# Kernel optimization log

Measured on AMD Instinct MI355X. Metric: run time of the kernel, lower is better.

## Reference

```python
import jax, jax.numpy as jnp
import numpy as np

S, D = 4096, 2048  # seq_len, embedding_space == qkv_dim


def setup_inputs() -> dict:
    key = jax.random.key(0)
    k1, k2, k3, k4, k5 = jax.random.split(key, 5)
    return {
        "input_embedding": jax.random.normal(k1, (S, D), dtype=jnp.float32),
        "query_embedding": jax.random.normal(k2, (S, D), dtype=jnp.float32),
        "Wq": jax.random.normal(k3, (D, D), dtype=jnp.float32) * 0.02,
        "Wk": jax.random.normal(k4, (D, D), dtype=jnp.float32) * 0.02,
        "Wv": jax.random.normal(k5, (D, D), dtype=jnp.float32) * 0.02,
        "include_mask": 0,  # False -> causal mask applied (module's inverted logic)
    }


def reference(input_embedding, query_embedding, Wq, Wk, Wv, include_mask):
    q = query_embedding @ Wq          # [S, D]
    k = input_embedding @ Wk          # [S, D]
    v = input_embedding @ Wv          # [S, D]
    scores = (q @ k.T) / 10.0         # [S, S]; module hardcodes /10, not sqrt(d)
    if not include_mask:
        # causal: -inf strictly above the diagonal (triu with offset 1)
        s = scores.shape[0]
        causal = jnp.tril(jnp.ones((s, s), dtype=bool))
        scores = jnp.where(causal, scores, -jnp.inf)
    probs = jax.nn.softmax(scores, axis=-1)
    return probs @ v                  # [S, D]
```

## Files before the change

kernel.cpp:

```cpp
#include <hip/hip_runtime.h>
#include <hip/hip_bf16.h>
#include <math.h>

typedef __bf16 bf16_t;
typedef __bf16 bf16x8 __attribute__((ext_vector_type(8)));
typedef float f32x4 __attribute__((ext_vector_type(4)));

enum { EP_BF16 = 0, EP_SCORES = 1, EP_F32 = 2 };

__device__ __forceinline__ void gload_lds16(const void* g, void* l) {
  __builtin_amdgcn_global_load_lds(
      (const __attribute__((address_space(1))) void*)g,
      (__attribute__((address_space(3))) void*)l, 16, 0, 0);
}


template <int TM, bool STG>
__device__ __forceinline__ void do_tile(char* smem, int slot, int sslot, size_t stoff,
                                        const char* const* gbase, const int* lbase,
                                        const int* aoff, const int* boff,
                                        f32x4 (&acc)[TM][4]) {
  bf16x8 bfr[4], af[4];
  if constexpr (TM == 8) {
    if constexpr (STG) {
      gload_lds16(gbase[0] + stoff, smem + sslot + lbase[0]);
      gload_lds16(gbase[1] + stoff, smem + sslot + lbase[1]);
    }
#pragma unroll
    for (int n = 0; n < 4; ++n) bfr[n] = *(const bf16x8*)(smem + slot + boff[n]);
#pragma unroll
    for (int m = 0; m < 4; ++m) af[m] = *(const bf16x8*)(smem + slot + aoff[m]);
    __builtin_amdgcn_s_setprio(1);
#pragma unroll
    for (int m = 0; m < 4; ++m)
#pragma unroll
      for (int n = 0; n < 4; ++n)
        acc[m][n] = __builtin_amdgcn_mfma_f32_16x16x32_bf16(af[m], bfr[n], acc[m][n], 0, 0, 0);
    __builtin_amdgcn_s_setprio(0);
    if constexpr (STG) __builtin_amdgcn_s_barrier();
    if constexpr (STG) {
      gload_lds16(gbase[2] + stoff, smem + sslot + lbase[2]);
      gload_lds16(gbase[3] + stoff, smem + sslot + lbase[3]);
    }
#pragma unroll
    for (int m = 0; m < 4; ++m) af[m] = *(const bf16x8*)(smem + slot + aoff[4 + m]);
    __builtin_amdgcn_s_setprio(1);
#pragma unroll
    for (int m = 0; m < 4; ++m)
#pragma unroll
      for (int n = 0; n < 4; ++n)
        acc[4 + m][n] = __builtin_amdgcn_mfma_f32_16x16x32_bf16(af[m], bfr[n], acc[4 + m][n], 0, 0, 0);
    __builtin_amdgcn_s_setprio(0);
  } else {
    if constexpr (STG) {
      gload_lds16(gbase[0] + stoff, smem + sslot + lbase[0]);
      gload_lds16(gbase[1] + stoff, smem + sslot + lbase[1]);
      gload_lds16(gbase[2] + stoff, smem + sslot + lbase[2]);
    }
#pragma unroll
    for (int n = 0; n < 4; ++n) bfr[n] = *(const bf16x8*)(smem + slot + boff[n]);
#pragma unroll
    for (int m = 0; m < 4; ++m) af[m] = *(const bf16x8*)(smem + slot + aoff[m]);
    __builtin_amdgcn_s_setprio(1);
#pragma unroll
    for (int m = 0; m < 4; ++m)
#pragma unroll
      for (int n = 0; n < 4; ++n)
        acc[m][n] = __builtin_amdgcn_mfma_f32_16x16x32_bf16(af[m], bfr[n], acc[m][n], 0, 0, 0);
    __builtin_amdgcn_s_setprio(0);
  }
}

template <int TM, int EPI>
__device__ __forceinline__ void gemm_core(
    const bf16_t* __restrict__ A, const bf16_t* __restrict__ B,
    void* __restrict__ Cout, int M, int N, int K,
    int row0, int col0, bool causal, float scale, char* smem)
{
  constexpr int BM = TM * 32;
  constexpr int LPT_A = BM / 128;
  constexpr int LPT = LPT_A + 2;
  constexpr int ABYTES = BM * 64;
  constexpr int SLOT = (BM + 256) * 64;

  const int tid = threadIdx.x;
  const int w = tid >> 6, lane = tid & 63;
  const int wr = w >> 2, wc = w & 3;

  int Keff = K;
  if (EPI == EP_F32 && causal) Keff = min(K, row0 + BM);
  const int nt = Keff >> 5;

  const char* gbase[LPT];
  int lbase[LPT];
  {
    const int sd = (tid & 3) ^ ((tid >> 3) & 3);
    const int rrow = tid >> 2;
#pragma unroll
    for (int r = 0; r < LPT; ++r) {
      const bool isA = (r < LPT_A);
      const int rr = isA ? r : (r - LPT_A);
      const int R = rr * 128 + rrow;
      const int grow = (isA ? row0 : col0) + R;
      const bf16_t* op = isA ? A : B;
      gbase[r] = (const char*)(op + (size_t)grow * K) + sd * 16;
      lbase[r] = (isA ? 0 : ABYTES) + rr * 8192 + w * 1024;
    }
  }

  const int fl = lane & 15;
  const int arow_off = fl * 64 + (((lane >> 4) ^ ((fl >> 1) & 3)) * 16);
  int aoff[TM], boff[4];
#pragma unroll
  for (int m = 0; m < TM; ++m) aoff[m] = (wr * (TM * 16) + m * 16) * 64 + arow_off;
#pragma unroll
  for (int n = 0; n < 4; ++n) boff[n] = ABYTES + (wc * 64 + n * 16) * 64 + arow_off;

  f32x4 acc[TM][4] = {};

  const int npro = nt < 3 ? nt : 3;
  for (int t = 0; t < npro; ++t)
#pragma unroll
    for (int r = 0; r < LPT; ++r)
      gload_lds16(gbase[r] + (size_t)t * 64, smem + (t & 3) * SLOT + lbase[r]);

  const int nmain = nt - 3;
  for (int t = 0; t < nmain; ++t) {
    if constexpr (TM == 8) asm volatile("s_waitcnt vmcnt(8)" ::: "memory");
    else                   asm volatile("s_waitcnt vmcnt(6)" ::: "memory");
    __builtin_amdgcn_s_barrier();
    asm volatile("" ::: "memory");
    __builtin_amdgcn_sched_barrier(0);
    do_tile<TM, true>(smem, (t & 3) * SLOT, ((t + 3) & 3) * SLOT,
                      (size_t)(t + 3) * 64, gbase, lbase, aoff, boff, acc);
  }

  asm volatile("s_waitcnt vmcnt(0)" ::: "memory");
  __builtin_amdgcn_s_barrier();
  asm volatile("" ::: "memory");
  __builtin_amdgcn_sched_barrier(0);
  for (int t = nmain > 0 ? nmain : 0; t < nt; ++t)
    do_tile<TM, false>(smem, (t & 3) * SLOT, 0, 0, gbase, lbase, aoff, boff, acc);

  const int cr = (lane >> 4) * 4;
  const int cc = lane & 15;
#pragma unroll
  for (int m = 0; m < TM; ++m) {
#pragma unroll
    for (int n = 0; n < 4; ++n) {
#pragma unroll
      for (int i = 0; i < 4; ++i) {
        const int r = row0 + wr * (TM * 16) + m * 16 + cr + i;
        const int c = col0 + wc * 64 + n * 16 + cc;
        float v = acc[m][n][i];
        if (EPI == EP_BF16) {
          ((bf16_t*)Cout)[(size_t)r * N + c] = (bf16_t)v;
        } else if (EPI == EP_SCORES) {
          v *= scale;
          if (causal && c > r) v = -INFINITY;
          ((float*)Cout)[(size_t)r * N + c] = v;
        } else {
          ((float*)Cout)[(size_t)r * N + c] = v;
        }
      }
    }
  }
}

template <int TM, int EPI>
__launch_bounds__(512, 2)
__global__ void gemm_k(const bf16_t* __restrict__ A, const bf16_t* __restrict__ B,
                       void* __restrict__ C, int M, int N, int K,
                       const int* __restrict__ maskflag, float scale) {
  extern __shared__ __align__(16) char smem[];
  const bool causal = (maskflag != nullptr) && (maskflag[0] == 0);
  constexpr int BM = TM * 32;
  const int ntn = N >> 8;
  const int wg = blockIdx.x;
  const int row0 = (wg / ntn) * BM, col0 = (wg % ntn) * 256;
  if (EPI == EP_SCORES && causal && col0 > row0 + BM - 1) return;
  gemm_core<TM, EPI>(A, B, C, M, N, K, row0, col0, causal, scale, smem);
}

__launch_bounds__(512, 2)
__global__ void qkv_k(const bf16_t* __restrict__ qe, const bf16_t* __restrict__ ie,
                      const bf16_t* __restrict__ WqT, const bf16_t* __restrict__ WkT,
                      const bf16_t* __restrict__ WvT,
                      bf16_t* __restrict__ q16, bf16_t* __restrict__ k16,
                      bf16_t* __restrict__ vT16) {
  extern __shared__ __align__(16) char smem[];
  int wg = blockIdx.x;
  const bf16_t *A, *B; bf16_t* C; int M, N;
  if (wg < 128)      { A = qe;  B = WqT; C = q16;  M = 4096; N = 2048; }
  else if (wg < 256) { A = ie;  B = WkT; C = k16;  M = 4096; N = 2048; wg -= 128; }
  else               { A = WvT; B = ie;  C = vT16; M = 2048; N = 4096; wg -= 256; }
  const int ntn = N >> 8;
  const int row0 = (wg / ntn) * 256, col0 = (wg % ntn) * 256;
  gemm_core<8, EP_BF16>(A, B, C, M, N, 2048, row0, col0, false, 1.f, smem);
}


__global__ void cvt_f32_bf16(const float* __restrict__ x, bf16_t* __restrict__ y, long n) {
  long i = ((long)blockIdx.x * blockDim.x + threadIdx.x) * 8;
  const long stride = (long)gridDim.x * blockDim.x * 8;
  for (; i < n; i += stride) {
    const float4 a = *(const float4*)(x + i);
    const float4 b = *(const float4*)(x + i + 4);
    bf16x8 o;
    o[0] = (__bf16)a.x; o[1] = (__bf16)a.y; o[2] = (__bf16)a.z; o[3] = (__bf16)a.w;
    o[4] = (__bf16)b.x; o[5] = (__bf16)b.y; o[6] = (__bf16)b.z; o[7] = (__bf16)b.w;
    *(bf16x8*)(y + i) = o;
  }
}

__global__ void transpose_cvt(const float* __restrict__ W, bf16_t* __restrict__ WT, int Dm) {
  __shared__ float tile[32][33];
  const int bx = blockIdx.x, by = blockIdx.y;
  const int tx = threadIdx.x & 31, ty = threadIdx.x >> 5;
#pragma unroll
  for (int r = ty; r < 32; r += 8)
    tile[r][tx] = W[(size_t)(by * 32 + r) * Dm + bx * 32 + tx];
  __syncthreads();
#pragma unroll
  for (int r = ty; r < 32; r += 8)
    WT[(size_t)(bx * 32 + r) * Dm + by * 32 + tx] = (bf16_t)tile[tx][r];
}

__global__ void softmax_rows(const float* __restrict__ Sc, bf16_t* __restrict__ P,
                             int n, const int* __restrict__ maskflag) {
  const int row = blockIdx.x;
  const int tid = threadIdx.x;
  const bool causal = maskflag[0] == 0;
  const int L = causal ? (row + 1) : n;
  const float* srow = Sc + (size_t)row * n;
  float v[16];
  float m = -INFINITY;
#pragma unroll
  for (int j = 0; j < 16; ++j) {
    const int idx = tid + j * 256;
    v[j] = (idx < L) ? srow[idx] : -INFINITY;
    m = fmaxf(m, v[j]);
  }
#pragma unroll
  for (int off = 32; off >= 1; off >>= 1) m = fmaxf(m, __shfl_xor(m, off));
  __shared__ float redm[4];
  __shared__ float reds[4];
  if ((tid & 63) == 0) redm[tid >> 6] = m;
  __syncthreads();
  m = fmaxf(fmaxf(redm[0], redm[1]), fmaxf(redm[2], redm[3]));
  float s = 0.f;
#pragma unroll
  for (int j = 0; j < 16; ++j) {
    v[j] = __expf(v[j] - m);
    s += v[j];
  }
#pragma unroll
  for (int off = 32; off >= 1; off >>= 1) s += __shfl_xor(s, off);
  if ((tid & 63) == 0) reds[tid >> 6] = s;
  __syncthreads();
  s = reds[0] + reds[1] + reds[2] + reds[3];
  const float inv = 1.f / s;
  bf16_t* prow = P + (size_t)row * n;
#pragma unroll
  for (int j = 0; j < 16; ++j) prow[tid + j * 256] = (bf16_t)(v[j] * inv);
}

extern "C" void kernel_launch(void* const* d_in, const int* in_sizes, int n_in,
                              void* d_out, int out_size, void* d_ws, size_t ws_size,
                              hipStream_t stream) {
  const float* ie = (const float*)d_in[0];
  const float* qe = (const float*)d_in[1];
  const float* Wq = (const float*)d_in[2];
  const float* Wk = (const float*)d_in[3];
  const float* Wv = (const float*)d_in[4];
  const int* mask = (const int*)d_in[5];
  float* out = (float*)d_out;

  const int S = 4096, D = 2048;
  char* ws = (char*)d_ws;
  const size_t MB = 1u << 20;
  bf16_t* q16  = (bf16_t*)(ws + 0 * MB);
  bf16_t* k16  = (bf16_t*)(ws + 16 * MB);
  bf16_t* vT16 = (bf16_t*)(ws + 32 * MB);
  bf16_t* qe16 = (bf16_t*)(ws + 48 * MB);
  bf16_t* ie16 = (bf16_t*)(ws + 64 * MB);
  bf16_t* WqT  = (bf16_t*)(ws + 80 * MB);
  bf16_t* WkT  = (bf16_t*)(ws + 88 * MB);
  bf16_t* WvT  = (bf16_t*)(ws + 96 * MB);
  float*  scores = (float*)(ws + 48 * MB);
  bf16_t* probs  = (bf16_t*)(ws + 112 * MB);

  hipFuncSetAttribute(reinterpret_cast<const void*>(&qkv_k),
                      hipFuncAttributeMaxDynamicSharedMemorySize, 131072);
  hipFuncSetAttribute(reinterpret_cast<const void*>(&gemm_k<8, EP_SCORES>),
                      hipFuncAttributeMaxDynamicSharedMemorySize, 131072);
  hipFuncSetAttribute(reinterpret_cast<const void*>(&gemm_k<4, EP_F32>),
                      hipFuncAttributeMaxDynamicSharedMemorySize, 98304);

  cvt_f32_bf16<<<2048, 256, 0, stream>>>(qe, qe16, (long)S * D);
  cvt_f32_bf16<<<2048, 256, 0, stream>>>(ie, ie16, (long)S * D);
  transpose_cvt<<<dim3(D / 32, D / 32), 256, 0, stream>>>(Wq, WqT, D);
  transpose_cvt<<<dim3(D / 32, D / 32), 256, 0, stream>>>(Wk, WkT, D);
  transpose_cvt<<<dim3(D / 32, D / 32), 256, 0, stream>>>(Wv, WvT, D);

  qkv_k<<<384, 512, 131072, stream>>>(qe16, ie16, WqT, WkT, WvT, q16, k16, vT16);

  gemm_k<8, EP_SCORES><<<256, 512, 131072, stream>>>(q16, k16, scores, S, S, D, mask, 0.1f);

  softmax_rows<<<S, 256, 0, stream>>>(scores, probs, S, mask);

  gemm_k<4, EP_F32><<<256, 512, 98304, stream>>>(probs, vT16, out, S, D, S, mask, 1.f);
}
```

Before: 289.8 us.

## Co-schedule V projection with causal score GEMM and swizzle workgroups across XCDs

Splits the fused QKV projection so Q and K are computed first, then runs the V projection in the same launch as the score GEMM. The score GEMM enumerates only the lower-triangular 256x256 tiles (136 instead of 256 launched blocks), and the combined launch is meant to fill the GPU better than a half-empty causal grid. Workgroup IDs are remapped so neighbouring tiles land on the same XCD for L2 reuse. The conversion and transpose launches are also merged into one launch each to cut launch overhead, and the workspace layout is rearranged so probs and scores can reuse buffers.

```diff
diff --git a/kernel.cpp b/kernel.cpp
--- a/kernel.cpp
+++ b/kernel.cpp
@@ -12,6 +12,11 @@
   __builtin_amdgcn_global_load_lds(
       (const __attribute__((address_space(1))) void*)g,
       (__attribute__((address_space(3))) void*)l, 16, 0, 0);
+}
+
+__device__ __forceinline__ int xcd_swz(int bid, int nwg) {
+  const int q = nwg >> 3;
+  return (bid & 7) * q + (bid >> 3);
 }
 
 
@@ -167,6 +172,47 @@
   }
 }
 
+__launch_bounds__(512, 2)
+__global__ void qk_k(const bf16_t* __restrict__ qe16, const bf16_t* __restrict__ ie16,
+                     const bf16_t* __restrict__ WqT, const bf16_t* __restrict__ WkT,
+                     bf16_t* __restrict__ q16, bf16_t* __restrict__ k16) {
+  extern __shared__ __align__(16) char smem[];
+  int wg = xcd_swz(blockIdx.x, gridDim.x);
+  const bf16_t *A, *B; bf16_t* C;
+  if (wg < 128) { A = qe16; B = WqT; C = q16; }
+  else          { A = ie16; B = WkT; C = k16; wg -= 128; }
+  const int row0 = (wg >> 3) * 256, col0 = (wg & 7) * 256;
+  gemm_core<8, EP_BF16>(A, B, C, 4096, 2048, 2048, row0, col0, false, 1.f, smem);
+}
+
+__launch_bounds__(512, 2)
+__global__ void vs_k(const bf16_t* __restrict__ WvT, const bf16_t* __restrict__ ie16,
+                     const bf16_t* __restrict__ q16, const bf16_t* __restrict__ k16,
+                     bf16_t* __restrict__ vT16, float* __restrict__ scores,
+                     const int* __restrict__ maskflag) {
+  extern __shared__ __align__(16) char smem[];
+  int wg = xcd_swz(blockIdx.x, gridDim.x);
+  if (wg < 128) {
+    const int row0 = (wg >> 4) * 256, col0 = (wg & 15) * 256;
+    gemm_core<8, EP_BF16>(WvT, ie16, vT16, 2048, 4096, 2048, row0, col0, false, 1.f, smem);
+  } else {
+    const int sid = wg - 128;
+    const bool causal = maskflag[0] == 0;
+    int r, c;
+    if (causal) {
+      if (sid >= 136) return;
+      r = (int)((sqrtf(8.f * (float)sid + 1.f) - 1.f) * 0.5f);
+      while ((r + 1) * (r + 2) / 2 <= sid) ++r;
+      while (r * (r + 1) / 2 > sid) --r;
+      c = sid - r * (r + 1) / 2;
+    } else {
+      r = sid >> 4; c = sid & 15;
+    }
+    gemm_core<8, EP_SCORES>(q16, k16, scores, 4096, 4096, 2048,
+                            r * 256, c * 256, causal, 0.1f, smem);
+  }
+}
+
 template <int TM, int EPI>
 __launch_bounds__(512, 2)
 __global__ void gemm_k(const bf16_t* __restrict__ A, const bf16_t* __restrict__ B,
@@ -176,31 +222,16 @@
   const bool causal = (maskflag != nullptr) && (maskflag[0] == 0);
   constexpr int BM = TM * 32;
   const int ntn = N >> 8;
-  const int wg = blockIdx.x;
+  const int wg = xcd_swz(blockIdx.x, gridDim.x);
   const int row0 = (wg / ntn) * BM, col0 = (wg % ntn) * 256;
-  if (EPI == EP_SCORES && causal && col0 > row0 + BM - 1) return;
   gemm_core<TM, EPI>(A, B, C, M, N, K, row0, col0, causal, scale, smem);
 }
 
-__launch_bounds__(512, 2)
-__global__ void qkv_k(const bf16_t* __restrict__ qe, const bf16_t* __restrict__ ie,
-                      const bf16_t* __restrict__ WqT, const bf16_t* __restrict__ WkT,
-                      const bf16_t* __restrict__ WvT,
-                      bf16_t* __restrict__ q16, bf16_t* __restrict__ k16,
-                      bf16_t* __restrict__ vT16) {
-  extern __shared__ __align__(16) char smem[];
-  int wg = blockIdx.x;
-  const bf16_t *A, *B; bf16_t* C; int M, N;
-  if (wg < 128)      { A = qe;  B = WqT; C = q16;  M = 4096; N = 2048; }
-  else if (wg < 256) { A = ie;  B = WkT; C = k16;  M = 4096; N = 2048; wg -= 128; }
-  else               { A = WvT; B = ie;  C = vT16; M = 2048; N = 4096; wg -= 256; }
-  const int ntn = N >> 8;
-  const int row0 = (wg / ntn) * 256, col0 = (wg % ntn) * 256;
-  gemm_core<8, EP_BF16>(A, B, C, M, N, 2048, row0, col0, false, 1.f, smem);
-}
-
-
-__global__ void cvt_f32_bf16(const float* __restrict__ x, bf16_t* __restrict__ y, long n) {
+
+__global__ void cvt_k(const float* __restrict__ qe, const float* __restrict__ ie,
+                      bf16_t* __restrict__ qe16, bf16_t* __restrict__ ie16, long n) {
+  const float* x = blockIdx.y ? ie : qe;
+  bf16_t* y = blockIdx.y ? ie16 : qe16;
   long i = ((long)blockIdx.x * blockDim.x + threadIdx.x) * 8;
   const long stride = (long)gridDim.x * blockDim.x * 8;
   for (; i < n; i += stride) {
@@ -213,7 +244,12 @@
   }
 }
 
-__global__ void transpose_cvt(const float* __restrict__ W, bf16_t* __restrict__ WT, int Dm) {
+__global__ void trans_k(const float* __restrict__ Wq, const float* __restrict__ Wk,
+                        const float* __restrict__ Wv,
+                        bf16_t* __restrict__ WqT, bf16_t* __restrict__ WkT,
+                        bf16_t* __restrict__ WvT, int Dm) {
+  const float* W = blockIdx.z == 0 ? Wq : (blockIdx.z == 1 ? Wk : Wv);
+  bf16_t* WT = blockIdx.z == 0 ? WqT : (blockIdx.z == 1 ? WkT : WvT);
   __shared__ float tile[32][33];
   const int bx = blockIdx.x, by = blockIdx.y;
   const int tx = threadIdx.x & 31, ty = threadIdx.x >> 5;
@@ -282,30 +318,27 @@
   bf16_t* q16  = (bf16_t*)(ws + 0 * MB);
   bf16_t* k16  = (bf16_t*)(ws + 16 * MB);
   bf16_t* vT16 = (bf16_t*)(ws + 32 * MB);
-  bf16_t* qe16 = (bf16_t*)(ws + 48 * MB);
-  bf16_t* ie16 = (bf16_t*)(ws + 64 * MB);
-  bf16_t* WqT  = (bf16_t*)(ws + 80 * MB);
-  bf16_t* WkT  = (bf16_t*)(ws + 88 * MB);
-  bf16_t* WvT  = (bf16_t*)(ws + 96 * MB);
-  float*  scores = (float*)(ws + 48 * MB);
-  bf16_t* probs  = (bf16_t*)(ws + 112 * MB);
-
-  hipFuncSetAttribute(reinterpret_cast<const void*>(&qkv_k),
+  bf16_t* ie16 = (bf16_t*)(ws + 48 * MB);
+  bf16_t* WvT  = (bf16_t*)(ws + 64 * MB);
+  bf16_t* qe16 = (bf16_t*)(ws + 72 * MB);
+  bf16_t* WqT  = (bf16_t*)(ws + 88 * MB);
+  bf16_t* WkT  = (bf16_t*)(ws + 96 * MB);
+  float*  scores = (float*)(ws + 72 * MB);
+  bf16_t* probs  = (bf16_t*)(ws + 0 * MB);
+
+  hipFuncSetAttribute(reinterpret_cast<const void*>(&qk_k),
                       hipFuncAttributeMaxDynamicSharedMemorySize, 131072);
-  hipFuncSetAttribute(reinterpret_cast<const void*>(&gemm_k<8, EP_SCORES>),
+  hipFuncSetAttribute(reinterpret_cast<const void*>(&vs_k),
                       hipFuncAttributeMaxDynamicSharedMemorySize, 131072);
   hipFuncSetAttribute(reinterpret_cast<const void*>(&gemm_k<4, EP_F32>),
                       hipFuncAttributeMaxDynamicSharedMemorySize, 98304);
 
-  cvt_f32_bf16<<<2048, 256, 0, stream>>>(qe, qe16, (long)S * D);
-  cvt_f32_bf16<<<2048, 256, 0, stream>>>(ie, ie16, (long)S * D);
-  transpose_cvt<<<dim3(D / 32, D / 32), 256, 0, stream>>>(Wq, WqT, D);
-  transpose_cvt<<<dim3(D / 32, D / 32), 256, 0, stream>>>(Wk, WkT, D);
-  transpose_cvt<<<dim3(D / 32, D / 32), 256, 0, stream>>>(Wv, WvT, D);
-
-  qkv_k<<<384, 512, 131072, stream>>>(qe16, ie16, WqT, WkT, WvT, q16, k16, vT16);
-
-  gemm_k<8, EP_SCORES><<<256, 512, 131072, stream>>>(q16, k16, scores, S, S, D, mask, 0.1f);
+  cvt_k<<<dim3(1024, 2), 256, 0, stream>>>(qe, ie, qe16, ie16, (long)S * D);
+  trans_k<<<dim3(D / 32, D / 32, 3), 256, 0, stream>>>(Wq, Wk, Wv, WqT, WkT, WvT, D);
+
+  qk_k<<<256, 512, 131072, stream>>>(qe16, ie16, WqT, WkT, q16, k16);
+
+  vs_k<<<384, 512, 131072, stream>>>(WvT, ie16, q16, k16, vT16, scores, mask);
 
   softmax_rows<<<S, 256, 0, stream>>>(scores, probs, S, mask);
 
```

New measurement: 294.8 us. About the same (+1.7%).
